# Kernel optimization log

Hardware: AMD Instinct MI355X
Metric: run time of the kernel (lower is better)

## Reference

```python
import jax, jax.numpy as jnp
import numpy as np
from jax import lax

B = 2048; T = 16; K = 12; G = T * B; NODES = G * (K + 1)
ENC = 64; GIN = 32; GHID = 64; GOUT = 32; EMB = 32; DEMB = 16
DYN = 32; DEC = 128; TOUT = 25; GRID = (13, 3); SCONV = 64; C31 = 16
SOC = ((GRID[0] - 4 + 1) // 2) * C31  # 80
TE = EMB * 3 + DEMB + GOUT            # 144


def _lstm(xs, Wih, Whh, bih, bhh):
    # xs: (T, N, in) seq-first, torch LSTM gate order i,f,g,o
    n = xs.shape[1]; H = Whh.shape[1]
    def step(carry, x):
        h, c = carry
        g = x @ Wih.T + h @ Whh.T + bih + bhh
        i, f, gg, o = jnp.split(g, 4, axis=-1)
        c = jax.nn.sigmoid(f) * c + jax.nn.sigmoid(i) * jnp.tanh(gg)
        h = jax.nn.sigmoid(o) * jnp.tanh(c)
        return (h, c), h
    z = jnp.zeros((n, H), xs.dtype)
    (h, _), hs = lax.scan(step, (z, z), xs)
    return hs, h


def _gat(x, src, dst, W, a_s, a_d, b, n):
    # PyG GATConv, heads=1, self-loops already in src/dst, leaky slope 0.2
    xw = x @ W.T
    e = jax.nn.leaky_relu((xw @ a_s)[src] + (xw @ a_d)[dst], 0.2)
    m = jax.ops.segment_max(e, dst, num_segments=n)
    ex = jnp.exp(e - m[dst])
    den = jax.ops.segment_sum(ex, dst, num_segments=n)
    alpha = ex / den[dst]
    return jax.ops.segment_sum(xw[src] * alpha[:, None], dst, num_segments=n) + b


def setup_inputs() -> dict:
    key = jax.random.key(0)
    ks = iter(jax.random.split(key, 80))
    f = lambda *s: jax.random.normal(next(ks), s, jnp.float32) * 0.05
    base = np.arange(G, dtype=np.int32) * (K + 1)          # ego node of each group
    nb = (base[:, None] + 1 + np.arange(K, dtype=np.int32)).reshape(-1)
    ego = np.repeat(base, K)
    edge_index = jnp.asarray(np.stack([np.concatenate([nb, ego]), np.concatenate([ego, nb])]))
    batch_gat = jnp.asarray(np.repeat(np.arange(G, dtype=np.int32), K + 1))
    m = np.zeros((B, GRID[1] * GRID[0], ENC), bool); m[:, :K, :] = True
    masks = jnp.asarray(m.reshape(B, GRID[1], GRID[0], ENC))
    return dict(
        data_figure_x=f(NODES, 4), edge_index=edge_index, batch_gat=batch_gat,
        hist=f(T, B, 2), hist_va=f(T, B, 2), hist_dis=f(T, B, 1), hist_lane=f(T, B, 2),
        nbrs=f(T, B * K, 2), nbrs_va=f(T, B * K, 2), nbrs_dis=f(T, B * K, 1), nbrs_lane=f(T, B * K, 2),
        masks=masks, lat_enc=f(B, 3), lon_enc=f(B, 2),
        ip_emb_W=f(GIN, 4), ip_emb_b=f(GIN),
        gat1_W=f(GHID, GIN), gat1_as=f(GHID), gat1_ad=f(GHID), gat1_b=f(GHID),
        gat2_W=f(GOUT, GHID), gat2_as=f(GOUT), gat2_ad=f(GOUT), gat2_b=f(GOUT),
        pos_W=f(EMB, 2), pos_b=f(EMB), va_W=f(EMB, 2), va_b=f(EMB),
        dis_W=f(DEMB, 1), dis_b=f(DEMB), lane_W=f(EMB, 2), lane_b=f(EMB),
        enc_Wih=f(4 * ENC, TE), enc_Whh=f(4 * ENC, ENC), enc_bih=f(4 * ENC), enc_bhh=f(4 * ENC),
        ta_Wih=f(4 * ENC, TE), ta_Whh=f(4 * ENC, ENC), ta_bih=f(4 * ENC), ta_bhh=f(4 * ENC),
        ta_TA_W=f(T, T * ENC), ta_TA_b=f(T),
        dyn_W=f(DYN, ENC), dyn_b=f(DYN),
        sconv_W=f(SCONV, ENC, 3, 3), sconv_b=f(SCONV),
        conv31_W=f(C31, SCONV, 3, 1), conv31_b=f(C31),
        dec_Wih=f(4 * DEC, 2 * SOC + DYN + 5), dec_Whh=f(4 * DEC, DEC), dec_bih=f(4 * DEC), dec_bhh=f(4 * DEC),
        op_W=f(5, DEC), op_b=f(5),
        oplat_W=f(3, 2 * SOC + DYN), oplat_b=f(3), oplon_W=f(2, 2 * SOC + DYN), oplon_b=f(2))


def reference(data_figure_x, edge_index, batch_gat, hist, hist_va, hist_dis, hist_lane,
              nbrs, nbrs_va, nbrs_dis, nbrs_lane, masks, lat_enc, lon_enc,
              ip_emb_W, ip_emb_b, gat1_W, gat1_as, gat1_ad, gat1_b,
              gat2_W, gat2_as, gat2_ad, gat2_b,
              pos_W, pos_b, va_W, va_b, dis_W, dis_b, lane_W, lane_b,
              enc_Wih, enc_Whh, enc_bih, enc_bhh,
              ta_Wih, ta_Whh, ta_bih, ta_bhh, ta_TA_W, ta_TA_b,
              dyn_W, dyn_b, sconv_W, sconv_b, conv31_W, conv31_b,
              dec_Wih, dec_Whh, dec_bih, dec_bhh, op_W, op_b,
              oplat_W, oplat_b, oplon_W, oplon_b):
    n = data_figure_x.shape[0]
    lrelu = lambda x: jax.nn.leaky_relu(x, 0.1)
    loop = jnp.arange(n, dtype=edge_index.dtype)
    src = jnp.concatenate([edge_index[0], loop])
    dst = jnp.concatenate([edge_index[1], loop])
    h = lrelu(data_figure_x @ ip_emb_W.T + ip_emb_b)
    h = lrelu(_gat(h, src, dst, gat1_W, gat1_as, gat1_ad, gat1_b, n))
    h = lrelu(_gat(h, src, dst, gat2_W, gat2_as, gat2_ad, gat2_b, n))
    # first node per group -> ego (hist), rest -> neighbors (batch_gat sorted)
    first_idx = jnp.searchsorted(batch_gat, jnp.arange(G, dtype=batch_gat.dtype))
    hist_gat = h[first_idx].reshape(T, B, GOUT)          # dropout = eval identity
    nbr_mask = jnp.ones(n, bool).at[first_idx].set(False)
    nbr_idx = jnp.where(nbr_mask, size=n - G)[0]
    nbrs_gat = h[nbr_idx].reshape(T, -1, GOUT)
    emb = lambda x, W, b: lrelu(x @ W.T + b)
    ch = jnp.concatenate([emb(hist, pos_W, pos_b), emb(hist_va, va_W, va_b),
                          emb(hist_dis, dis_W, dis_b), emb(hist_lane, lane_W, lane_b), hist_gat], -1)
    cn = jnp.concatenate([emb(nbrs, pos_W, pos_b), emb(nbrs_va, va_W, va_b),
                          emb(nbrs_dis, dis_W, dis_b), emb(nbrs_lane, lane_W, lane_b), nbrs_gat], -1)
    # TA_LSTM: temporal attention over per-step hidden states
    hs, _ = _lstm(ch, ta_Wih, ta_Whh, ta_bih, ta_bhh)     # (T, B, ENC)
    total = hs.transpose(1, 0, 2).reshape(B, T * ENC)
    beta = jax.nn.softmax(jax.nn.relu(total @ ta_TA_W.T + ta_TA_b), axis=-1)
    hist_enc = lrelu(jnp.einsum('tbh,bt->bh', hs, beta) @ dyn_W.T + dyn_b)
    _, nbrs_enc = _lstm(cn, enc_Wih, enc_Whh, enc_bih, enc_bhh)   # (B*K, ENC)
    # masked_scatter_: fill True positions row-major with flattened nbrs_enc
    mflat = masks.reshape(-1)
    sidx = jnp.clip(jnp.cumsum(mflat) - 1, 0)
    soc = jnp.where(mflat, nbrs_enc.reshape(-1)[sidx], 0.0).reshape(masks.shape).astype(jnp.float32)
    soc = soc.transpose(0, 3, 2, 1)                       # (B, ENC, 13, 3)
    dn = ('NCHW', 'OIHW', 'NCHW')
    soc = lrelu(lax.conv_general_dilated(soc, sconv_W, (1, 1), 'VALID', dimension_numbers=dn)
                + sconv_b[None, :, None, None])
    soc = lrelu(lax.conv_general_dilated(soc, conv31_W, (1, 1), 'VALID', dimension_numbers=dn)
                + conv31_b[None, :, None, None])          # (B, C31, 9, 1)
    pad = ((0, 0), (0, 0), (1, 1), (0, 0))
    mx = lax.reduce_window(soc, -jnp.inf, lax.max, (1, 1, 2, 1), (1, 1, 2, 1), pad).reshape(-1, SOC)
    av = (lax.reduce_window(soc, 0.0, lax.add, (1, 1, 2, 1), (1, 1, 2, 1), pad) / 2.0).reshape(-1, SOC)
    enc = jnp.concatenate([mx, av, hist_enc], 1)          # (B, 2*SOC+DYN)
    lat_pred = jax.nn.softmax(enc @ oplat_W.T + oplat_b, axis=1)
    lon_pred = jax.nn.softmax(enc @ oplon_W.T + oplon_b, axis=1)
    encd = jnp.concatenate([enc, lat_enc, lon_enc], 1)
    rep = jnp.broadcast_to(encd[None], (TOUT,) + encd.shape)
    hs2, _ = _lstm(rep, dec_Wih, dec_Whh, dec_bih, dec_bhh)
    fut = hs2 @ op_W.T + op_b                             # (TOUT, B, 5)
    out = jnp.concatenate([fut[..., 0:2], jnp.exp(fut[..., 2:4]), jnp.tanh(fut[..., 4:5])], -1)
    return out, lat_pred, lon_pred
```

## Files before the change

kernel.cpp:

```cpp
#include <hip/hip_runtime.h>
#include <hip/hip_bf16.h>
#include <cstddef>
#include <cstdint>
#include <math.h>

typedef __hip_bfloat16 bf16;
typedef _Float16 f16;
typedef _Float16 f16x8 __attribute__((ext_vector_type(8)));
typedef _Float16 f16x2 __attribute__((ext_vector_type(2)));
typedef float f32x4 __attribute__((ext_vector_type(4)));
#define MFMA16(a,b,c) __builtin_amdgcn_mfma_f32_16x16x32_f16(a,b,c,0,0,0)

#define DEV __device__ __forceinline__
DEV float bff(bf16 x){ return __bfloat162float(x); }
DEV bf16 fbf(float x){ return __float2bfloat16(x); }
DEV float lr01(float x){ return x>0.f? x : 0.1f*x; }
DEV float lr02(float x){ return x>0.f? x : 0.2f*x; }
DEV float frcp(float x){ return __builtin_amdgcn_rcpf(x); }
DEV float sigm(float x){ return frcp(1.f+__expf(-x)); }
DEV float tanhe(float x){ float a=fabsf(x); float e=__expf(-2.f*a); float t=(1.f-e)*frcp(1.f+e); return x<0.f? -t : t; }
DEV void stout(void* out, int isf, size_t i, float v){
  if (isf) ((float*)out)[i] = v; else ((bf16*)out)[i] = fbf(v);
}
DEV float bfu_lo(unsigned u){ return __uint_as_float(u << 16); }
DEV float bfu_hi(unsigned u){ return __uint_as_float(u & 0xffff0000u); }
DEV float ldr(const void* p, size_t i, int isf){
  return isf ? ((const float*)p)[i] : bff(((const bf16*)p)[i]);
}

#define NBATCH 2048
#define TSEQ 16
#define KNB 12
#define NGRP 32768
#define NNODES 425984
#define NBK 24576
#define NTOUT 25

__global__ __launch_bounds__(256) void detect_k(const uint32_t* __restrict__ x, int* __restrict__ flag) {
  __shared__ int cnt;
  if (threadIdx.x == 0) cnt = 0;
  __syncthreads();
  float v = __uint_as_float(x[threadIdx.x]);
  float a = fabsf(v);
  if (a > 1e-12f && a < 100.f) atomicAdd(&cnt, 1);
  __syncthreads();
  if (threadIdx.x == 0) *flag = (cnt >= 128) ? 1 : 0;
}

#define NCVT 55
struct CvtArgs {
  const void* src[NCVT];
  unsigned off[NCVT];
  unsigned cnt[NCVT];
};

__global__ __launch_bounds__(256) void cvtprep_k(CvtArgs a, float* __restrict__ dst,
    const int* __restrict__ flag, unsigned total,
    const void* __restrict__ scW, const void* __restrict__ c31W,
    const void* __restrict__ g1W, const void* __restrict__ g2W,
    const void* __restrict__ encWhh, const void* __restrict__ taWhh,
    const void* __restrict__ decWhh,
    f16* __restrict__ wp1t, f16* __restrict__ wp2t,
    float* __restrict__ w1t, float* __restrict__ w2t,
    f16* __restrict__ wench, f16* __restrict__ wtah, f16* __restrict__ wdech) {
  const int isf = *flag;
  if (blockIdx.x < 4096) {
    for (size_t e = (size_t)blockIdx.x*256 + threadIdx.x; e < total; e += (size_t)4096*256) {
      int lo = 0, hi = NCVT-1;
      while (lo < hi) { int mid = (lo+hi+1)>>1; if ((size_t)a.off[mid] <= e) lo = mid; else hi = mid-1; }
      unsigned r = (unsigned)(e - a.off[lo]);
      float v = isf ? ((const float*)a.src[lo])[r] : bff(((const bf16*)a.src[lo])[r]);
      dst[e] = v;
    }
    return;
  }
  int idx = (blockIdx.x - 4096)*256 + threadIdx.x;
  if (idx < 12288) {
    int o = idx & 63; int k = idx >> 6; int kh = k >> 6; int i = k & 63;
    wp1t[idx] = (f16)ldr(scW, ((size_t)(o*64+i)*3 + kh)*3, isf);
  } else if (idx < 15360) {
    int e = idx - 12288;
    int o = e & 15; int k = e >> 4; int kh = k >> 6; int i = k & 63;
    wp2t[e] = (f16)ldr(c31W, (size_t)(o*64+i)*3 + kh, isf);
  } else if (idx < 17408) {
    int e = idx - 15360; int k = e >> 6, f = e & 63;
    w1t[e] = ldr(g1W, f*32 + k, isf);
  } else if (idx < 19456) {
    int e = idx - 17408; int k = e >> 5, f = e & 31;
    w2t[e] = ldr(g2W, f*64 + k, isf);
  } else if (idx < 35840) {
    int e = idx - 19456;
    wench[e] = (f16)ldr(encWhh, e, isf);
  } else if (idx < 52224) {
    int e = idx - 35840;
    wtah[e] = (f16)ldr(taWhh, e, isf);
  } else if (idx < 117760) {
    int e = idx - 52224;
    wdech[e] = (f16)ldr(decWhh, e, isf);
  }
}

__global__ __launch_bounds__(256) void gat_dense1_k(const float* __restrict__ x,
    const float* __restrict__ ipW, const float* __restrict__ ipb,
    const float* __restrict__ Wt, const float* __restrict__ as_, const float* __restrict__ ad_,
    bf16* __restrict__ out, float* __restrict__ esed) {
  __shared__ float As[64][33];
  __shared__ float Ws[32][64];
  __shared__ float xs[64][4];
  __shared__ float wipw[128];
  __shared__ float wipb[32];
  const int tid = threadIdx.x;
  const size_t bm = (size_t)blockIdx.x * 64;
  ((float*)xs)[tid] = x[bm*4 + tid];
  if (tid < 128) wipw[tid] = ipW[tid];
  else if (tid < 160) wipb[tid-128] = ipb[tid-128];
  #pragma unroll
  for (int i = 0; i < 8; i++) ((float*)Ws)[tid + 256*i] = Wt[tid + 256*i];
  __syncthreads();
  #pragma unroll
  for (int i = 0; i < 8; i++) {
    int e = tid + 256*i; int v = e >> 5, f = e & 31;
    float a = wipb[f];
    #pragma unroll
    for (int k = 0; k < 4; k++) a += xs[v][k]*wipw[f*4+k];
    As[v][f] = lr01(a);
  }
  __syncthreads();
  const int v = tid >> 2, f0 = (tid & 3) * 16;
  float acc[16];
  #pragma unroll
  for (int i = 0; i < 16; i++) acc[i] = 0.f;
  #pragma unroll 8
  for (int k = 0; k < 32; k++) {
    float a = As[v][k];
    const float4* wr = (const float4*)&Ws[k][f0];
    #pragma unroll
    for (int q = 0; q < 4; q++) {
      float4 w4 = wr[q];
      acc[4*q+0] += a*w4.x; acc[4*q+1] += a*w4.y; acc[4*q+2] += a*w4.z; acc[4*q+3] += a*w4.w;
    }
  }
  bf16* op = out + (bm+v)*64 + f0;
  #pragma unroll
  for (int i = 0; i < 16; i++) op[i] = fbf(acc[i]);
  float es = 0.f, ed = 0.f;
  #pragma unroll
  for (int i = 0; i < 16; i++) { es += acc[i]*as_[f0+i]; ed += acc[i]*ad_[f0+i]; }
  es += __shfl_xor(es, 1); es += __shfl_xor(es, 2);
  ed += __shfl_xor(ed, 1); ed += __shfl_xor(ed, 2);
  if ((tid & 3) == 0) { esed[(bm+v)*2] = es; esed[(bm+v)*2+1] = ed; }
}

__global__ __launch_bounds__(256) void gat_dense2_k(const bf16* __restrict__ in,
    const float* __restrict__ Wt, const float* __restrict__ as_, const float* __restrict__ ad_,
    bf16* __restrict__ out, float* __restrict__ esed) {
  __shared__ float As[64][65];
  __shared__ float Ws[64][32];
  const int tid = threadIdx.x;
  const size_t bm = (size_t)blockIdx.x * 64;
  #pragma unroll
  for (int i = 0; i < 16; i++) {
    int lin = tid + 256*i;
    As[lin>>6][lin&63] = bff(in[bm*64 + lin]);
    if (i < 8) ((float*)Ws)[tid + 256*i] = Wt[tid + 256*i];
  }
  __syncthreads();
  const int v = tid >> 2, f0 = (tid & 3) * 8;
  float acc[8];
  #pragma unroll
  for (int i = 0; i < 8; i++) acc[i] = 0.f;
  #pragma unroll 8
  for (int k = 0; k < 64; k++) {
    float a = As[v][k];
    const float4* wr = (const float4*)&Ws[k][f0];
    #pragma unroll
    for (int q = 0; q < 2; q++) {
      float4 w4 = wr[q];
      acc[4*q+0] += a*w4.x; acc[4*q+1] += a*w4.y; acc[4*q+2] += a*w4.z; acc[4*q+3] += a*w4.w;
    }
  }
  bf16* op = out + (bm+v)*32 + f0;
  #pragma unroll
  for (int i = 0; i < 8; i++) op[i] = fbf(acc[i]);
  float es = 0.f, ed = 0.f;
  #pragma unroll
  for (int i = 0; i < 8; i++) { es += acc[i]*as_[f0+i]; ed += acc[i]*ad_[f0+i]; }
  es += __shfl_xor(es, 1); es += __shfl_xor(es, 2);
  ed += __shfl_xor(ed, 1); ed += __shfl_xor(ed, 2);
  if ((tid & 3) == 0) { esed[(bm+v)*2] = es; esed[(bm+v)*2+1] = ed; }
}

__global__ __launch_bounds__(256) void alpha_k(const float* __restrict__ esed, float* __restrict__ alph) {
  int g = blockIdx.x*256 + threadIdx.x;
  size_t base = (size_t)g*13;
  float esv[13], edv[13];
  #pragma unroll
  for (int i = 0; i < 13; i++) { esv[i] = esed[(base+i)*2]; edv[i] = esed[(base+i)*2+1]; }
  float* o = alph + (size_t)g*40;
  float e[13]; float m = -1e30f;
  #pragma unroll
  for (int i = 0; i < 13; i++) { float z = lr02(esv[i] + edv[0]); e[i] = z; m = fmaxf(m, z); }
  float den = 0.f;
  #pragma unroll
  for (int i = 0; i < 13; i++) { e[i] = __expf(e[i]-m); den += e[i]; }
  float inv = 1.f/den;
  #pragma unroll
  for (int i = 0; i < 13; i++) o[i] = e[i]*inv;
  #pragma unroll
  for (int j = 1; j <= 12; j++) {
    float z0 = lr02(esv[0] + edv[j]);
    float z1 = lr02(esv[j] + edv[j]);
    float mm = fmaxf(z0, z1);
    float a0 = __expf(z0-mm), a1 = __expf(z1-mm);
    float s = 1.f/(a0+a1);
    o[13 + 2*(j-1)] = a0*s;
    o[14 + 2*(j-1)] = a1*s;
  }
}

template<int F>
__global__ __launch_bounds__(256) void agg8_k(const bf16* __restrict__ xw, const float* __restrict__ alph,
                                              const float* __restrict__ bias, bf16* __restrict__ out) {
  const int NV = F/8;
  size_t idx = (size_t)blockIdx.x*256 + threadIdx.x;
  int f8 = (int)(idx % NV);
  size_t vn = idx / NV;
  int node = (int)(vn % 13);
  size_t g = vn / 13;
  size_t base = g*13;
  const float* al = alph + g*40;
  const int f0 = f8*8;
  float acc[8];
  if (node == 0) {
    #pragma unroll
    for (int j = 0; j < 8; j++) acc[j] = 0.f;
    #pragma unroll
    for (int i = 0; i < 13; i++) {
      const uint4 rv = *(const uint4*)&xw[(base+i)*F + f0];
      float a = al[i];
      acc[0] += a*bfu_lo(rv.x); acc[1] += a*bfu_hi(rv.x);
      acc[2] += a*bfu_lo(rv.y); acc[3] += a*bfu_hi(rv.y);
      acc[4] += a*bfu_lo(rv.z); acc[5] += a*bfu_hi(rv.z);
      acc[6] += a*bfu_lo(rv.w); acc[7] += a*bfu_hi(rv.w);
    }
  } else {
    float a0 = al[13 + 2*(node-1)], a1 = al[14 + 2*(node-1)];
    const uint4 r0v = *(const uint4*)&xw[base*F + f0];
    const uint4 r1v = *(const uint4*)&xw[(base+node)*F + f0];
    acc[0] = a0*bfu_lo(r0v.x) + a1*bfu_lo(r1v.x);
    acc[1] = a0*bfu_hi(r0v.x) + a1*bfu_hi(r1v.x);
    acc[2] = a0*bfu_lo(r0v.y) + a1*bfu_lo(r1v.y);
    acc[3] = a0*bfu_hi(r0v.y) + a1*bfu_hi(r1v.y);
    acc[4] = a0*bfu_lo(r0v.z) + a1*bfu_lo(r1v.z);
    acc[5] = a0*bfu_hi(r0v.z) + a1*bfu_hi(r1v.z);
    acc[6] = a0*bfu_lo(r0v.w) + a1*bfu_lo(r1v.w);
    acc[7] = a0*bfu_hi(r0v.w) + a1*bfu_hi(r1v.w);
  }
  bf16* op = out + vn*F + f0;
  #pragma unroll
  for (int j = 0; j < 8; j++) op[j] = fbf(lr01(acc[j] + bias[f0+j]));
}

template<bool NBR>
__global__ __launch_bounds__(256) void gemm_embed_mfma_k(
    const float* __restrict__ p_in, const float* __restrict__ v_in,
    const float* __restrict__ di_in, const float* __restrict__ l_in,
    const bf16* __restrict__ h2,
    const float* __restrict__ posW, const float* __restrict__ posb,
    const float* __restrict__ vaW, const float* __restrict__ vab,
    const float* __restrict__ disW, const float* __restrict__ disb,
    const float* __restrict__ laneW, const float* __restrict__ laneb,
    const float* __restrict__ W, f16* __restrict__ C, int t0) {
  __shared__ __align__(16) f16 As[128][40];
  __shared__ __align__(16) f16 Bs[128][40];
  const int tid = threadIdx.x;
  const int bm = blockIdx.x * 128, bn = blockIdx.y * 128;
  const int bz = blockIdx.z;
  const int mm = tid & 127, par = tid >> 7;
  int t, n2;
  if (NBR) { t = t0 + bz; n2 = bm + mm; }
  else { int gm = bm + mm; t = gm >> 11; n2 = gm & 2047; }
  const int NROW = NBR ? NBK : NBATCH;
  size_t rn = (size_t)t*NROW + n2;
  const float px0 = p_in[rn*2], px1 = p_in[rn*2+1];
  const float vx0 = v_in[rn*2], vx1 = v_in[rn*2+1];
  const float dx  = di_in[rn];
  const float lx0 = l_in[rn*2], lx1 = l_in[rn*2+1];
  const int b = NBR ? (n2 / KNB) : n2;
  const int node_off = NBR ? (1 + n2 % KNB) : 0;
  const bf16* h2p = h2 + (((size_t)t*NBATCH + b)*13 + node_off)*32;
  const int wn = bn + mm;
  const int l = tid & 63, wv = tid >> 6;
  const int lr = l & 15, lq = l >> 4;
  f32x4 acc[2][8];
  #pragma unroll
  for (int rt = 0; rt < 2; rt++)
    #pragma unroll
    for (int ct = 0; ct < 8; ct++) acc[rt][ct] = (f32x4){0.f,0.f,0.f,0.f};
  for (int ks = 0; ks < 5; ks++) {
    const int k0 = ks*32;
    #pragma unroll
    for (int e = 0; e < 16; e++) {
      int kk = par + 2*e;
      int f = k0 + kk;
      float val;
      if (f < 32) {
        val = lr01(px0*posW[f*2] + px1*posW[f*2+1] + posb[f]);
      } else if (f < 64) {
        int ff = f-32;
        val = lr01(vx0*vaW[ff*2] + vx1*vaW[ff*2+1] + vab[ff]);
      } else if (f < 80) {
        int ff = f-64;
        val = lr01(dx*disW[ff] + disb[ff]);
      } else if (f < 112) {
        int ff = f-80;
        val = lr01(lx0*laneW[ff*2] + lx1*laneW[ff*2+1] + laneb[ff]);
      } else if (f < 144) {
        val = bff(h2p[f-112]);
      } else val = 0.f;
      As[mm][kk] = (f16)val;
      Bs[mm][kk] = (f < 144) ? (f16)W[(size_t)wn*144 + f] : (f16)0.f;
    }
    __syncthreads();
    f16x8 a0 = *(const f16x8*)&As[wv*32 + lr][lq*8];
    f16x8 a1 = *(const f16x8*)&As[wv*32 + 16 + lr][lq*8];
    #pragma unroll
    for (int ct = 0; ct < 8; ct++) {
      f16x8 bfr = *(const f16x8*)&Bs[ct*16 + lr][lq*8];
      acc[0][ct] = MFMA16(a0, bfr, acc[0][ct]);
      acc[1][ct] = MFMA16(a1, bfr, acc[1][ct]);
    }
    __syncthreads();
  }
  #pragma unroll
  for (int rt = 0; rt < 2; rt++)
    #pragma unroll
    for (int ct = 0; ct < 8; ct++)
      #pragma unroll
      for (int rg = 0; rg < 4; rg++) {
        int row = wv*32 + rt*16 + lq*4 + rg;
        int col = ct*16 + lr;
        size_t orow = NBR ? ((size_t)bz*NBK + bm + row) : (size_t)(bm + row);
        C[orow*256 + bn + col] = (f16)acc[rt][ct][rg];
      }
}

__global__ __launch_bounds__(512, 4) void enc_ta_mega_k(
    const float* __restrict__ p_in, const float* __restrict__ v_in,
    const float* __restrict__ di_in, const float* __restrict__ l_in,
    const bf16* __restrict__ h2,
    const float* __restrict__ posW, const float* __restrict__ posb,
    const float* __restrict__ vaW, const float* __restrict__ vab,
    const float* __restrict__ disW, const float* __restrict__ disb,
    const float* __restrict__ laneW, const float* __restrict__ laneb,
    const float* __restrict__ Wih, const f16* __restrict__ Whh16,
    const float* __restrict__ bih, const float* __restrict__ bhh,
    float* __restrict__ hstate,
    const f16* __restrict__ XWta, const f16* __restrict__ Whh16ta,
    const float* __restrict__ bihta, const float* __restrict__ bhhta,
    float* __restrict__ h_all_ta) {
  __shared__ __align__(16) union SMem {
    struct { f16 As_s[2][16][168]; f16 h_s[2][16][72]; float gates[16][258]; } e;
    struct { f16 h_s[16][72]; float gates[16][260]; } a;
  } sm;
  const int tid = threadIdx.x;
  const int l = tid & 63;
  const int lr = l & 15, lq = l >> 4;

  if (blockIdx.x < 128) {
    const int r0 = blockIdx.x * 16;
    const int wv = tid >> 6;
    const int u = l, rg = wv;
    f16x8 bf[4][2];
    if (wv < 4) {
      #pragma unroll
      for (int ct = 0; ct < 4; ct++)
        #pragma unroll
        for (int kt = 0; kt < 2; kt++)
          bf[ct][kt] = *(const f16x8*)&Whh16ta[(size_t)(wv*64 + ct*16 + lr)*64 + kt*32 + lq*8];
    }
    float bj4[4];
    #pragma unroll
    for (int g = 0; g < 4; g++) bj4[g] = bihta[g*64+u] + bhhta[g*64+u];
    for (int i = tid; i < 16*64; i += 512) sm.a.h_s[i>>6][i&63] = (f16)0.f;
    float c[4] = {0.f,0.f,0.f,0.f};
    __syncthreads();
    #pragma unroll 1
    for (int s = 0; s < TSEQ; s++) {
      if (wv < 4) {
        f16x8 a0 = *(const f16x8*)&sm.a.h_s[lr][lq*8];
        f16x8 a1 = *(const f16x8*)&sm.a.h_s[lr][32 + lq*8];
        f32x4 acc[4];
        #pragma unroll
        for (int ct = 0; ct < 4; ct++) {
          acc[ct] = (f32x4){0.f,0.f,0.f,0.f};
          acc[ct] = MFMA16(a0, bf[ct][0], acc[ct]);
          acc[ct] = MFMA16(a1, bf[ct][1], acc[ct]);
        }
        #pragma unroll
        for (int ct = 0; ct < 4; ct++)
          #pragma unroll
          for (int q2 = 0; q2 < 4; q2++)
            sm.a.gates[lq*4 + q2][wv*64 + ct*16 + lr] = acc[ct][q2];
      }
      __syncthreads();
      if (wv < 4) {
        const f16* xwrow = XWta + ((size_t)s*NBATCH + r0)*256;
        #pragma unroll
        for (int q = 0; q < 4; q++) {
          const int r = rg*4 + q;
          float gi = sm.a.gates[r][u]     + bj4[0] + (float)xwrow[(size_t)r*256 + u];
          float gf = sm.a.gates[r][64+u]  + bj4[1] + (float)xwrow[(size_t)r*256 + 64 + u];
          float gg = sm.a.gates[r][128+u] + bj4[2] + (float)xwrow[(size_t)r*256 + 128 + u];
          float go = sm.a.gates[r][192+u] + bj4[3] + (float)xwrow[(size_t)r*256 + 192 + u];
          float cv = sigm(gf)*c[q] + sigm(gi)*tanhe(gg);
          c[q] = cv;
          float hv = sigm(go)*tanhe(cv);
          sm.a.h_s[r][u] = (f16)hv;
          h_all_ta[((size_t)s*NBATCH + r0 + r)*64 + u] = hv;
        }
      }
      __syncthreads();
    }
    return;
  }

  const int r0 = (blockIdx.x - 128) * 16;
  const int w = tid >> 6;
  const int cu0 = w*16 + lr;
  const int cu1 = 128 + cu0;
  f16x8 bxw[2][5];
  f16x8 bhw[2][2];
  float bv[2];
  #pragma unroll
  for (int s = 0; s < 2; s++) {
    const int cu = s ? cu1 : cu0;
    const float* wr = Wih + (size_t)cu*144;
    #pragma unroll
    for (int ks = 0; ks < 5; ks++) {
      f16x8 v;
      #pragma unroll
      for (int j = 0; j < 8; j++) {
        int k = ks*32 + lq*8 + j;
        v[j] = (k < 144) ? (f16)wr[k] : (f16)0.f;
      }
      bxw[s][ks] = v;
    }
    #pragma unroll
    for (int kt = 0; kt < 2; kt++)
      bhw[s][kt] = *(const f16x8*)&Whh16[(size_t)cu*64 + kt*32 + lq*8];
    bv[s] = bih[cu] + bhh[cu];
  }
  const int prow = tid & 15;
  const int pq = tid >> 4;
  const int n2 = r0 + prow;
  const int bb = n2 / KNB;
  const int noff = 1 + n2 - bb*KNB;
  float c0 = 0.f, c1 = 0.f;
  float La = 0.f, Lb = 0.f;
  uint4 HA = {0,0,0,0};
  for (int i = tid; i < 16*64; i += 512) sm.e.h_s[0][i>>6][i&63] = (f16)0.f;

#define ENC_ISSUE(TP) do {                                                   \
    const size_t rnp = (size_t)(TP)*NBK + n2;                                \
    if (pq < 4)       { float2 p = *(const float2*)(p_in + rnp*2); La = p.x; Lb = p.y; } \
    else if (pq < 8)  { float2 p = *(const float2*)(v_in + rnp*2); La = p.x; Lb = p.y; } \
    else if (pq < 10) { La = di_in[rnp]; }                                   \
    else if (pq < 14) { float2 p = *(const float2*)(l_in + rnp*2); La = p.x; Lb = p.y; } \
    else if (pq < 18) { HA = *(const uint4*)(h2 + (((size_t)(TP)*NBATCH + bb)*13 + noff)*32 + (pq-14)*8); } \
  } while (0)

#define ENC_STAGE(BUF) do {                                                  \
    if (pq < 20) {                                                           \
      const int f0 = pq*8;                                                   \
      f16x8 v;                                                               \
      if (f0 < 32) {                                                         \
        _Pragma("unroll")                                                    \
        for (int j = 0; j < 8; j++)                                          \
          v[j] = (f16)lr01(La*posW[(f0+j)*2] + Lb*posW[(f0+j)*2+1] + posb[f0+j]); \
      } else if (f0 < 64) {                                                  \
        _Pragma("unroll")                                                    \
        for (int j = 0; j < 8; j++) {                                        \
          int ff = f0+j-32;                                                  \
          v[j] = (f16)lr01(La*vaW[ff*2] + Lb*vaW[ff*2+1] + vab[ff]);         \
        }                                                                    \
      } else if (f0 < 80) {                                                  \
        _Pragma("unroll")                                                    \
        for (int j = 0; j < 8; j++) {                                        \
          int ff = f0+j-64;                                                  \
          v[j] = (f16)lr01(La*disW[ff] + disb[ff]);                          \
        }                                                                    \
      } else if (f0 < 112) {                                                 \
        _Pragma("unroll")                                                    \
        for (int j = 0; j < 8; j++) {                                        \
          int ff = f0+j-80;                                                  \
          v[j] = (f16)lr01(La*laneW[ff*2] + Lb*laneW[ff*2+1] + laneb[ff]);   \
        }                                                                    \
      } else if (f0 < 144) {                                                 \
        v[0] = (f16)bfu_lo(HA.x); v[1] = (f16)bfu_hi(HA.x);                  \
        v[2] = (f16)bfu_lo(HA.y); v[3] = (f16)bfu_hi(HA.y);                  \
        v[4] = (f16)bfu_lo(HA.z); v[5] = (f16)bfu_hi(HA.z);                  \
        v[6] = (f16)bfu_lo(HA.w); v[7] = (f16)bfu_hi(HA.w);                  \
      } else {                                                               \
        _Pragma("unroll")                                                    \
        for (int j = 0; j < 8; j++) v[j] = (f16)0.f;                         \
      }                                                                      \
      *(f16x8*)&sm.e.As_s[BUF][prow][f0] = v;                                \
    }                                                                        \
  } while (0)

  ENC_ISSUE(0);
  ENC_STAGE(0);
  __syncthreads();
  int cur = 0;
  #pragma unroll 1
  for (int t = 0; t < TSEQ; t++) {
    const int tp = (t+1 < TSEQ) ? t+1 : t;
    ENC_ISSUE(tp);
    {
      f16x8 ae0 = *(const f16x8*)&sm.e.As_s[cur][lr][lq*8];
      f16x8 ae1 = *(const f16x8*)&sm.e.As_s[cur][lr][32 + lq*8];
      f16x8 ae2 = *(const f16x8*)&sm.e.As_s[cur][lr][64 + lq*8];
      f16x8 ae3 = *(const f16x8*)&sm.e.As_s[cur][lr][96 + lq*8];
      f16x8 ae4 = *(const f16x8*)&sm.e.As_s[cur][lr][128 + lq*8];
      f16x8 ah0 = *(const f16x8*)&sm.e.h_s[cur][lr][lq*8];
      f16x8 ah1 = *(const f16x8*)&sm.e.h_s[cur][lr][32 + lq*8];
      #pragma unroll
      for (int s = 0; s < 2; s++) {
        f32x4 a = (f32x4){0.f,0.f,0.f,0.f};
        a = MFMA16(ae0, bxw[s][0], a);
        a = MFMA16(ae1, bxw[s][1], a);
        a = MFMA16(ae2, bxw[s][2], a);
        a = MFMA16(ae3, bxw[s][3], a);
        a = MFMA16(ae4, bxw[s][4], a);
        a = MFMA16(ah0, bhw[s][0], a);
        a = MFMA16(ah1, bhw[s][1], a);
        const int cu = s ? cu1 : cu0;
        #pragma unroll
        for (int q = 0; q < 4; q++)
          sm.e.gates[lq*4 + q][cu] = a[q] + bv[s];
      }
    }
    __syncthreads();
    {
      const int u0 = pq*2;
      const float* gr = &sm.e.gates[prow][0];
      float gi0 = gr[u0],       gi1 = gr[u0+1];
      float gf0 = gr[64+u0],    gf1 = gr[64+u0+1];
      float gg0 = gr[128+u0],   gg1 = gr[128+u0+1];
      float go0 = gr[192+u0],   go1 = gr[192+u0+1];
      float cv0 = sigm(gf0)*c0 + sigm(gi0)*tanhe(gg0);
      float cv1 = sigm(gf1)*c1 + sigm(gi1)*tanhe(gg1);
      c0 = cv0; c1 = cv1;
      f16x2 hv;
      hv[0] = (f16)(sigm(go0)*tanhe(cv0));
      hv[1] = (f16)(sigm(go1)*tanhe(cv1));
      *(f16x2*)&sm.e.h_s[cur^1][prow][u0] = hv;
    }
    ENC_STAGE(cur^1);
    __syncthreads();
    cur ^= 1;
  }
#undef ENC_ISSUE
#undef ENC_STAGE
  for (int i = tid; i < 16*64; i += 512)
    hstate[(size_t)(r0 + (i>>6))*64 + (i&63)] = (float)sm.e.h_s[cur][i>>6][i&63];
}

__global__ __launch_bounds__(256, 2) void head_k(const bf16* __restrict__ A, const float* __restrict__ W,
    float* __restrict__ C, int N, int Kd,
    const float* __restrict__ e192,
    const float* __restrict__ latW, const float* __restrict__ latb,
    const float* __restrict__ lonW, const float* __restrict__ lonb,
    void* __restrict__ out, const int* __restrict__ flag) {
  const int tid = threadIdx.x;
  if (blockIdx.x < 64) {
    __shared__ __align__(16) float As[8][132];
    __shared__ __align__(16) float Bs[8][132];
    const int bm = (blockIdx.x >> 2) * 128, bn = (blockIdx.x & 3) * 128;
    const int tx = tid & 15, ty = tid >> 4;
    float acc[8][8];
    #pragma unroll
    for (int i = 0; i < 8; i++)
      #pragma unroll
      for (int j = 0; j < 8; j++) acc[i][j] = 0.f;
    for (int k0 = 0; k0 < Kd; k0 += 8) {
      #pragma unroll
      for (int i = 0; i < 4; i++) {
        int lin = tid + 256*i;
        int kk = lin & 7, mm = lin >> 3;
        int gk = k0 + kk;
        As[kk][mm] = (gk < Kd) ? bff(A[(size_t)(bm+mm)*Kd + gk]) : 0.f;
        Bs[kk][mm] = (gk < Kd) ? W[(size_t)(bn+mm)*Kd + gk] : 0.f;
      }
      __syncthreads();
      #pragma unroll
      for (int kk = 0; kk < 8; kk++) {
        float4 a0 = *(const float4*)&As[kk][ty*4];
        float4 a1 = *(const float4*)&As[kk][64+ty*4];
        float4 b0 = *(const float4*)&Bs[kk][tx*4];
        float4 b1 = *(const float4*)&Bs[kk][64+tx*4];
        float av[8] = {a0.x,a0.y,a0.z,a0.w,a1.x,a1.y,a1.z,a1.w};
        float bvv[8] = {b0.x,b0.y,b0.z,b0.w,b1.x,b1.y,b1.z,b1.w};
        #pragma unroll
        for (int i = 0; i < 8; i++)
          #pragma unroll
          for (int j = 0; j < 8; j++) acc[i][j] += av[i]*bvv[j];
      }
      __syncthreads();
    }
    #pragma unroll
    for (int i = 0; i < 8; i++) {
      int m = bm + (i>>2)*64 + ty*4 + (i&3);
      #pragma unroll
      for (int jh = 0; jh < 2; jh++) {
        float4 v = make_float4(acc[i][jh*4+0], acc[i][jh*4+1], acc[i][jh*4+2], acc[i][jh*4+3]);
        *(float4*)&C[(size_t)m*N + bn + jh*64 + tx*4] = v;
      }
    }
  } else {
    int b = (blockIdx.x - 64)*256 + tid;
    const int isf = *flag;
    const float* e = e192 + (size_t)b*192;
    float s[3];
    #pragma unroll
    for (int c2 = 0; c2 < 3; c2++) {
      float acc = latb[c2];
      for (int k = 0; k < 192; k++) acc += e[k]*latW[c2*192+k];
      s[c2] = acc;
    }
    float m = fmaxf(s[0], fmaxf(s[1], s[2]));
    float e0 = __expf(s[0]-m), e1 = __expf(s[1]-m), e2 = __expf(s[2]-m);
    float inv = 1.f/(e0+e1+e2);
    stout(out, isf, 256000 + (size_t)b*3 + 0, e0*inv);
    stout(out, isf, 256000 + (size_t)b*3 + 1, e1*inv);
    stout(out, isf, 256000 + (size_t)b*3 + 2, e2*inv);
    float q[2];
    #pragma unroll
    for (int c2 = 0; c2 < 2; c2++) {
      float acc = lonb[c2];
      for (int k = 0; k < 192; k++) acc += e[k]*lonW[c2*192+k];
      q[c2] = acc;
    }
    float m2 = fmaxf(q[0], q[1]);
    float f0 = __expf(q[0]-m2), f1 = __expf(q[1]-m2);
    float inv2 = 1.f/(f0+f1);
    stout(out, isf, 262144 + (size_t)b*2 + 0, f0*inv2);
    stout(out, isf, 262144 + (size_t)b*2 + 1, f1*inv2);
  }
}

__global__ __launch_bounds__(512) void lstm128_out_k(const float* __restrict__ XW,
    const f16* __restrict__ Whh16, const float* __restrict__ bih, const float* __restrict__ bhh,
    int steps, const float* __restrict__ opW, const float* __restrict__ opb,
    void* __restrict__ out, const int* __restrict__ flag) {
  __shared__ __align__(16) f16 h_s[2][16][136];
  __shared__ float hsf[2][16][132];
  __shared__ float opWs[640];
  __shared__ float opbs[5];
  const int tid = threadIdx.x;
  const int r0 = blockIdx.x * 16;
  const int l = tid & 63, wv = tid >> 6;
  const int lr = l & 15, lq = l >> 4;
  const int u = wv*16 + lr;
  const int isf = *flag;
  f16x8 bf[4][4];
  #pragma unroll
  for (int g = 0; g < 4; g++)
    #pragma unroll
    for (int kt = 0; kt < 4; kt++)
      bf[g][kt] = *(const f16x8*)&Whh16[(size_t)(g*128 + u)*128 + kt*32 + lq*8];
  float xr[4][4];
  #pragma unroll
  for (int g = 0; g < 4; g++) {
    float bj = bih[g*128 + u] + bhh[g*128 + u];
    #pragma unroll
    for (int rg = 0; rg < 4; rg++)
      xr[g][rg] = XW[(size_t)(r0 + lq*4 + rg)*512 + g*128 + u] + bj;
  }
  for (int i = tid; i < 16*128; i += 512) h_s[0][i>>7][i&127] = (f16)0.f;
  for (int i = tid; i < 640; i += 512) opWs[i] = opW[i];
  if (tid < 5) opbs[tid] = opb[tid];
  float c[4] = {0.f,0.f,0.f,0.f};
  __syncthreads();
  int cur = 0;
  #pragma unroll 1
  for (int t = 0; t < steps; t++) {
    f16x8 a0 = *(const f16x8*)&h_s[cur][lr][lq*8];
    f16x8 a1 = *(const f16x8*)&h_s[cur][lr][32 + lq*8];
    f16x8 a2 = *(const f16x8*)&h_s[cur][lr][64 + lq*8];
    f16x8 a3 = *(const f16x8*)&h_s[cur][lr][96 + lq*8];
    f32x4 acc[4];
    #pragma unroll
    for (int g = 0; g < 4; g++) {
      acc[g] = (f32x4){0.f,0.f,0.f,0.f};
      acc[g] = MFMA16(a0, bf[g][0], acc[g]);
      acc[g] = MFMA16(a1, bf[g][1], acc[g]);
      acc[g] = MFMA16(a2, bf[g][2], acc[g]);
      acc[g] = MFMA16(a3, bf[g][3], acc[g]);
    }
    #pragma unroll
    for (int rg = 0; rg < 4; rg++) {
      const int row = lq*4 + rg;
      float gi = acc[0][rg] + xr[0][rg];
      float gf = acc[1][rg] + xr[1][rg];
      float gg = acc[2][rg] + xr[2][rg];
      float go = acc[3][rg] + xr[3][rg];
      float cv = sigm(gf)*c[rg] + sigm(gi)*tanhe(gg);
      c[rg] = cv;
      float hv = sigm(go)*tanhe(cv);
      h_s[cur^1][row][u] = (f16)hv;
      hsf[cur^1][row][u] = hv;
    }
    __syncthreads();
    if (tid < 80) {
      const int row = tid / 5, c2 = tid - (tid/5)*5;
      float acc2 = opbs[c2];
      const float* hr = &hsf[cur^1][row][0];
      for (int k = 0; k < 128; k++) acc2 += hr[k]*opWs[c2*128+k];
      size_t oidx = ((size_t)t*NBATCH + r0 + row)*5 + c2;
      float v = (c2 < 2) ? acc2 : (c2 < 4 ? __expf(acc2) : tanhe(acc2));
      stout(out, isf, oidx, v);
    }
    cur ^= 1;
  }
}

__global__ __launch_bounds__(256) void ta_fused_k(const float* __restrict__ hs,
    const float* __restrict__ W, const float* __restrict__ bias,
    const float* __restrict__ dynW, const float* __restrict__ dynb,
    float* __restrict__ henc) {
  __shared__ float hsl[8][1024];
  __shared__ float scl[8][16];
  const int tid = threadIdx.x;
  const int b0 = blockIdx.x * 8;
  for (int i = tid; i < 8*1024; i += 256) {
    int bb = i >> 10, r = i & 1023;
    int t = r >> 6, h = r & 63;
    hsl[bb][r] = hs[((size_t)t*NBATCH + b0 + bb)*64 + h];
  }
  __syncthreads();
  if (tid < 128) {
    int bb = tid >> 4, i = tid & 15;
    float acc = bias[i];
    for (int t = 0; t < 16; t++) {
      const float* hr = &hsl[bb][t*64];
      const float* wr = W + (size_t)i*1024 + t*64;
      #pragma unroll
      for (int h = 0; h < 64; h++) acc += hr[h]*wr[h];
    }
    scl[bb][i] = fmaxf(acc, 0.f);
  }
  __syncthreads();
  {
    int bb = tid >> 5, o = tid & 31;
    const float* s = scl[bb];
    float m = s[0];
    #pragma unroll
    for (int t = 1; t < 16; t++) m = fmaxf(m, s[t]);
    float e[16]; float den = 0.f;
    #pragma unroll
    for (int t = 0; t < 16; t++) { e[t] = __expf(s[t]-m); den += e[t]; }
    float inv = 1.f/den;
    float acc = dynb[o];
    for (int t = 0; t < 16; t++) {
      const float* hr = &hsl[bb][t*64];
      float inner = 0.f;
      #pragma unroll
      for (int h = 0; h < 64; h++) inner += hr[h]*dynW[(size_t)o*64 + h];
      acc += (e[t]*inv)*inner;
    }
    henc[(size_t)(b0+bb)*32 + o] = lr01(acc);
  }
}

__global__ __launch_bounds__(256) void fused_conv_k(const float* __restrict__ nenc,
    const f16* __restrict__ wp1t, const f16* __restrict__ wp2t,
    const float* __restrict__ scb, const float* __restrict__ c31b,
    const float* __restrict__ henc, const float* __restrict__ lat_enc, const float* __restrict__ lon_enc,
    float* __restrict__ e192, bf16* __restrict__ encd) {
  __shared__ f16 ws1[12288];
  __shared__ f16 ws2[3072];
  __shared__ float img[4][13][64];
  __shared__ float c1s[4][64][12];
  __shared__ float c2s[4][16][9];
  const int tid = threadIdx.x;
  const int l = tid & 63, wv = tid >> 6;
  const int b = blockIdx.x*4 + wv;
  #pragma unroll
  for (int it = 0; it < 24; it++) ((uint32_t*)ws1)[tid + 256*it] = ((const uint32_t*)wp1t)[tid + 256*it];
  #pragma unroll
  for (int it = 0; it < 6; it++) ((uint32_t*)ws2)[tid + 256*it] = ((const uint32_t*)wp2t)[tid + 256*it];
  #pragma unroll
  for (int it = 0; it < 13; it++)
    img[wv][it][l] = (it < 12) ? nenc[((size_t)b*12 + it)*64 + l] : 0.f;
  __syncthreads();
  {
    const int o = l;
    float acc[11];
    float bv = scb[o];
    #pragma unroll
    for (int h = 0; h < 11; h++) acc[h] = bv;
    for (int k = 0; k < 192; k++) {
      int kh = k >> 6, i = k & 63;
      float w = (float)ws1[k*64 + o];
      const float* ic = img[wv][kh];
      #pragma unroll
      for (int h = 0; h < 11; h++) acc[h] += ic[h*64 + i] * w;
    }
    #pragma unroll
    for (int h = 0; h < 11; h++) c1s[wv][o][h] = lr01(acc[h]);
  }
  __syncthreads();
  if (l < 48) {
    const int o2 = l / 3, jg = l - o2*3;
    float acc[3];
    float bv = c31b[o2];
    #pragma unroll
    for (int m = 0; m < 3; m++) acc[m] = bv;
    for (int k = 0; k < 192; k++) {
      int kh = k >> 6, i = k & 63;
      float w = (float)ws2[k*16 + o2];
      #pragma unroll
      for (int m = 0; m < 3; m++) acc[m] += c1s[wv][i][jg*3 + m + kh] * w;
    }
    #pragma unroll
    for (int m = 0; m < 3; m++) c2s[wv][o2][jg*3 + m] = lr01(acc[m]);
  }
  __syncthreads();
  for (int it = 0; it < 4; it++) {
    int k = l + it*64;
    if (k >= 197) break;
    float val;
    if (k < 192) {
      if (k < 160) {
        bool is_av = (k >= 80);
        int rel = is_av ? (k - 80) : k;
        int o = rel / 5, p = rel - o*5;
        const float* r = c2s[wv][o];
        float v2 = r[2*p];
        if (p == 0) val = is_av ? v2*0.5f : v2;
        else { float v1 = r[2*p-1]; val = is_av ? (v1+v2)*0.5f : fmaxf(v1, v2); }
      } else {
        val = henc[(size_t)b*32 + (k-160)];
      }
      e192[(size_t)b*192 + k] = val;
    } else if (k < 195) {
      val = lat_enc[(size_t)b*3 + (k-192)];
    } else {
      val = lon_enc[(size_t)b*2 + (k-195)];
    }
    encd[(size_t)b*197 + k] = fbf(val);
  }
}

static const size_t OFF_H2   = 0;
static const size_t OFF_P    = 6815744;
static const size_t OFF_Q    = 20447232;
static const size_t OFF_ESED = 34078720;
static const size_t OFF_ALPH = 34930688;
static const size_t OFF_XWTA = 6815744;
static const size_t OFF_HSTA = 15204352;
static const size_t OFF_HST  = 23691264;
static const size_t OFF_E192 = 28573696;
static const size_t OFF_ENCD = 28966912;
static const size_t OFF_XWD  = 29168640;
static const size_t OFF_HEN  = 35000000;
static const size_t OFF_CVT  = 36241408;
static const size_t OFF_WP1T = 41280000;
static const size_t OFF_WP2T = 41286144;
static const size_t OFF_W1T  = 41287680;
static const size_t OFF_W2T  = 41289728;
static const size_t OFF_WENC = 41291776;
static const size_t OFF_WTAH = 41299968;
static const size_t OFF_WDECH= 41308160;
static const size_t OFF_FLAG = 41400000;

extern "C" void kernel_launch(void* const* d_in, const int* in_sizes, int n_in,
                              void* d_out, int out_size, void* d_ws, size_t ws_size,
                              hipStream_t stream) {
  (void)in_sizes; (void)n_in; (void)out_size; (void)ws_size;
  float* ws = (float*)d_ws;
  int* flag = (int*)(ws + OFF_FLAG);

  static const int   cidx[NCVT] = {0,3,4,5,6,7,8,9,10,12,13,
    14,15,16,17,18,19,20,21,22,23,24,25,26,27,28,29,30,31,
    32,33,34,35,36,37,38,39,40,41,42,43,44,45,46,47,
    48,49,50,51,52,53,54,55,56,57};
  static const unsigned ccnt[NCVT] = {1703936,65536,65536,32768,65536,786432,786432,393216,786432,6144,4096,
    128,32,2048,64,64,64,2048,32,32,32,64,32,64,32,16,16,64,32,
    36864,16384,256,256,36864,16384,256,256,16384,16,2048,32,36864,64,3072,16,
    100864,65536,512,512,640,5,576,3,384,2};
  CvtArgs ca;
  unsigned total = 0;
  float* cp[58];
  for (int i = 0; i < NCVT; i++) {
    ca.src[i] = d_in[cidx[i]];
    ca.off[i] = total;
    ca.cnt[i] = ccnt[i];
    cp[cidx[i]] = ws + OFF_CVT + total;
    total += ccnt[i];
  }
  detect_k<<<1,256,0,stream>>>((const uint32_t*)d_in[0], flag);

  void* out = d_out;
  bf16*  h2    = (bf16*)(ws + OFF_H2);
  bf16*  h1    = (bf16*)(ws + OFF_P);
  bf16*  xw1   = (bf16*)(ws + OFF_Q);
  bf16*  xw2   = (bf16*)(ws + OFF_Q);
  float* esed  = ws + OFF_ESED;
  float* alph  = ws + OFF_ALPH;
  f16*   xwta  = (f16*)(ws + OFF_XWTA);
  float* hsta  = ws + OFF_HSTA;
  float* henc  = ws + OFF_HEN;
  float* hst   = ws + OFF_HST;
  float* e192  = ws + OFF_E192;
  bf16*  encd  = (bf16*)(ws + OFF_ENCD);
  float* xwd   = ws + OFF_XWD;
  f16*   wp1t  = (f16*)(ws + OFF_WP1T);
  f16*   wp2t  = (f16*)(ws + OFF_WP2T);
  float* w1t   = ws + OFF_W1T;
  float* w2t   = ws + OFF_W2T;
  f16*   wench = (f16*)(ws + OFF_WENC);
  f16*   wtah  = (f16*)(ws + OFF_WTAH);
  f16*   wdech = (f16*)(ws + OFF_WDECH);

  cvtprep_k<<<4556,256,0,stream>>>(ca, ws + OFF_CVT, flag, total,
      d_in[44], d_in[46], d_in[16], d_in[20], d_in[33], d_in[37], d_in[49],
      wp1t, wp2t, w1t, w2t, wench, wtah, wdech);

  gat_dense1_k<<<6656,256,0,stream>>>(cp[0], cp[14], cp[15], w1t, cp[17], cp[18], xw1, esed);
  alpha_k<<<128,256,0,stream>>>(esed, alph);
  agg8_k<64><<<13312,256,0,stream>>>(xw1, alph, cp[19], h1);
  gat_dense2_k<<<6656,256,0,stream>>>(h1, w2t, cp[21], cp[22], xw2, esed);
  alpha_k<<<128,256,0,stream>>>(esed, alph);
  agg8_k<32><<<6656,256,0,stream>>>(xw2, alph, cp[23], h2);

  gemm_embed_mfma_k<false><<<dim3(256,2,1),256,0,stream>>>(cp[3], cp[4], cp[5], cp[6], h2,
      cp[24],cp[25],cp[26],cp[27],cp[28],cp[29],cp[30],cp[31], cp[36], xwta, 0);

  enc_ta_mega_k<<<1664,512,0,stream>>>(cp[7], cp[8], cp[9], cp[10], h2,
      cp[24],cp[25],cp[26],cp[27],cp[28],cp[29],cp[30],cp[31],
      cp[32], wench, cp[34], cp[35], hst,
      xwta, wtah, cp[38], cp[39], hsta);

  ta_fused_k<<<256,256,0,stream>>>(hsta, cp[40], cp[41], cp[42], cp[43], henc);

  fused_conv_k<<<512,256,0,stream>>>(hst, wp1t, wp2t, cp[45], cp[47], henc, cp[12], cp[13], e192, encd);

  head_k<<<72,256,0,stream>>>(encd, cp[48], xwd, 512, 197,
      e192, cp[54], cp[55], cp[56], cp[57], out, flag);

  lstm128_out_k<<<128,512,0,stream>>>(xwd, wdech, cp[50], cp[51], NTOUT,
      cp[52], cp[53], out, flag);
}
```

Baseline: 717.1 us.

## Fuse first GAT aggregation into second GAT dense projection kernel

The layer-1 attention aggregation (bias, leaky ReLU, bf16 rounding) now runs inside the layer-2 dense kernel while it loads its input tile. The separate agg8 launch and the h1 intermediate buffer are gone. This removes one kernel launch and a full write and read of h1 through global memory. In exchange, ego rows gather all 13 neighbor rows and are imbalanced against leaf rows, and xw2 moves to a different workspace buffer.

```diff
diff --git a/kernel.cpp b/kernel.cpp
--- a/kernel.cpp
+++ b/kernel.cpp
@@ -151,7 +151,8 @@
   if ((tid & 3) == 0) { esed[(bm+v)*2] = es; esed[(bm+v)*2+1] = ed; }
 }
 
-__global__ __launch_bounds__(256) void gat_dense2_k(const bf16* __restrict__ in,
+__global__ __launch_bounds__(256) void gat_dense2_k(const bf16* __restrict__ xw1,
+    const float* __restrict__ alph, const float* __restrict__ bias1,
     const float* __restrict__ Wt, const float* __restrict__ as_, const float* __restrict__ ad_,
     bf16* __restrict__ out, float* __restrict__ esed) {
   __shared__ float As[64][65];
@@ -159,10 +160,46 @@
   const int tid = threadIdx.x;
   const size_t bm = (size_t)blockIdx.x * 64;
   #pragma unroll
-  for (int i = 0; i < 16; i++) {
-    int lin = tid + 256*i;
-    As[lin>>6][lin&63] = bff(in[bm*64 + lin]);
-    if (i < 8) ((float*)Ws)[tid + 256*i] = Wt[tid + 256*i];
+  for (int i = 0; i < 8; i++) ((float*)Ws)[tid + 256*i] = Wt[tid + 256*i];
+  #pragma unroll
+  for (int it = 0; it < 2; it++) {
+    const int grp = tid + 256*it;
+    const int node = grp >> 3;
+    const int f0 = (grp & 7) * 8;
+    const size_t nid = bm + node;
+    const size_t g = nid / 13;
+    const int r = (int)(nid - g*13);
+    const size_t base = g*13;
+    const float* al = alph + g*40;
+    float acc[8];
+    if (r == 0) {
+      #pragma unroll
+      for (int j = 0; j < 8; j++) acc[j] = 0.f;
+      #pragma unroll
+      for (int i = 0; i < 13; i++) {
+        const uint4 rv = *(const uint4*)&xw1[(base+i)*64 + f0];
+        float a = al[i];
+        acc[0] += a*bfu_lo(rv.x); acc[1] += a*bfu_hi(rv.x);
+        acc[2] += a*bfu_lo(rv.y); acc[3] += a*bfu_hi(rv.y);
+        acc[4] += a*bfu_lo(rv.z); acc[5] += a*bfu_hi(rv.z);
+        acc[6] += a*bfu_lo(rv.w); acc[7] += a*bfu_hi(rv.w);
+      }
+    } else {
+      float a0 = al[13 + 2*(r-1)], a1 = al[14 + 2*(r-1)];
+      const uint4 r0v = *(const uint4*)&xw1[base*64 + f0];
+      const uint4 r1v = *(const uint4*)&xw1[(base+r)*64 + f0];
+      acc[0] = a0*bfu_lo(r0v.x) + a1*bfu_lo(r1v.x);
+      acc[1] = a0*bfu_hi(r0v.x) + a1*bfu_hi(r1v.x);
+      acc[2] = a0*bfu_lo(r0v.y) + a1*bfu_lo(r1v.y);
+      acc[3] = a0*bfu_hi(r0v.y) + a1*bfu_hi(r1v.y);
+      acc[4] = a0*bfu_lo(r0v.z) + a1*bfu_lo(r1v.z);
+      acc[5] = a0*bfu_hi(r0v.z) + a1*bfu_hi(r1v.z);
+      acc[6] = a0*bfu_lo(r0v.w) + a1*bfu_lo(r1v.w);
+      acc[7] = a0*bfu_hi(r0v.w) + a1*bfu_hi(r1v.w);
+    }
+    #pragma unroll
+    for (int j = 0; j < 8; j++)
+      As[node][f0+j] = bff(fbf(lr01(acc[j] + bias1[f0+j])));
   }
   __syncthreads();
   const int v = tid >> 2, f0 = (tid & 3) * 8;
@@ -905,9 +942,8 @@
 
   void* out = d_out;
   bf16*  h2    = (bf16*)(ws + OFF_H2);
-  bf16*  h1    = (bf16*)(ws + OFF_P);
   bf16*  xw1   = (bf16*)(ws + OFF_Q);
-  bf16*  xw2   = (bf16*)(ws + OFF_Q);
+  bf16*  xw2   = (bf16*)(ws + OFF_P);
   float* esed  = ws + OFF_ESED;
   float* alph  = ws + OFF_ALPH;
   f16*   xwta  = (f16*)(ws + OFF_XWTA);
@@ -931,8 +967,7 @@
 
   gat_dense1_k<<<6656,256,0,stream>>>(cp[0], cp[14], cp[15], w1t, cp[17], cp[18], xw1, esed);
   alpha_k<<<128,256,0,stream>>>(esed, alph);
-  agg8_k<64><<<13312,256,0,stream>>>(xw1, alph, cp[19], h1);
-  gat_dense2_k<<<6656,256,0,stream>>>(h1, w2t, cp[21], cp[22], xw2, esed);
+  gat_dense2_k<<<6656,256,0,stream>>>(xw1, alph, cp[19], w2t, cp[21], cp[22], xw2, esed);
   alpha_k<<<128,256,0,stream>>>(esed, alph);
   agg8_k<32><<<6656,256,0,stream>>>(xw2, alph, cp[23], h2);
 
```

Result: faster. 687.2 us (-4.2%).
